# Optimization experiments

Hardware: AMD Instinct MI355X
Metric: run time of the kernel (lower is better)

The kernel has to match this reference:

```python
import jax, jax.numpy as jnp
import numpy as np
import math

H = 14
W = 14
MU_MAX = math.sqrt((H / 2) ** 2 + (W / 2) ** 2)
EPS = 1e-6
LN_EPS = 1e-5


def _distance_sq():
    fy = np.fft.fftfreq(H) * H
    fx = np.fft.rfftfreq(W) * W
    d = fy[:, None] ** 2 + fx[None, :] ** 2  # (H, W//2+1)
    return jnp.asarray(d[None, None], dtype=jnp.float32)  # (1,1,H,W//2+1)


def setup_inputs() -> dict:
    key = jax.random.key(0)
    k0, k1, k2 = jax.random.split(key, 3)
    B, C, HID = 256, 768, 192  # hidden = max(768//4, 8)
    return {
        "x": jax.random.normal(k0, (B, 197, C), jnp.float32),
        "ln_gamma": jnp.ones((C,), jnp.float32),
        "ln_beta": jnp.zeros((C,), jnp.float32),
        "w1": jax.random.normal(k1, (C, HID), jnp.float32) * 0.02,
        "b1": jnp.zeros((HID,), jnp.float32),
        "w2": jax.random.normal(k2, (HID, 2), jnp.float32) * 0.02,
        "b2": jnp.zeros((2,), jnp.float32),
        "residual_scale": jnp.asarray(1e-4, jnp.float32),
    }


def reference(x, ln_gamma, ln_beta, w1, b1, w2, b2, residual_scale):
    b, _, c = x.shape
    cls_tok = x[:, :1]          # (B,1,C)
    xs = x[:, 1:]               # (B,196,C) raw spatial tokens
    # LayerNorm (biased variance, eps=1e-5 like torch default)
    mu_ln = xs.mean(-1, keepdims=True)
    var_ln = xs.var(-1, keepdims=True)
    xn = (xs - mu_ln) / jnp.sqrt(var_ln + LN_EPS) * ln_gamma + ln_beta
    # to (B,C,H,W) grid
    xg = xn.transpose(0, 2, 1).reshape(b, c, H, W)
    xm = xg.mean((-2, -1), keepdims=True)
    spec = jnp.fft.rfft2(xg - xm, norm='ortho')  # (B,C,H,W//2+1) complex
    energy = jnp.log1p(jnp.abs(spec)).mean((-2, -1))  # (B,C)
    hdn = jax.nn.gelu(energy @ w1 + b1, approximate=False)
    out2 = hdn @ w2 + b2  # (B,2)
    mu = jnp.maximum(MU_MAX * jax.nn.sigmoid(out2[:, 0]), 1.0).reshape(b, 1, 1, 1)
    sigma = jnp.maximum(jax.nn.softplus(out2[:, 1]), 0.1).reshape(b, 1, 1, 1)
    mask = jnp.exp(-_distance_sq() / (2.0 * mu ** 2 * sigma + EPS))
    filtered = jnp.fft.irfft2(spec * mask, s=(H, W), norm='ortho') + xm
    toks = filtered.reshape(b, c, H * W).transpose(0, 2, 1)  # (B,196,C)
    delta = toks - xn
    return jnp.concatenate([cls_tok, xs + residual_scale * delta], axis=1)
```

## Files before the change

kernel.cpp:

```cpp
#include <hip/hip_runtime.h>
#include <hip/hip_fp16.h>
#include <math.h>

#define NB    256
#define NTOKP 197
#define NTOK  196
#define NC    768
#define NHID  192
#define NH    14
#define NVF   8
#define CHT   64
#define NTILE 12
#define NCH   8
#define CCH   (NC / NCH)

constexpr float CT14[14] = {
    1.0f, 0.9009688679024191f, 0.6234898018587336f, 0.22252093395631445f,
    -0.22252093395631434f, -0.6234898018587335f, -0.9009688679024191f, -1.0f,
    -0.9009688679024191f, -0.6234898018587335f, -0.22252093395631434f,
    0.22252093395631445f, 0.6234898018587336f, 0.9009688679024191f};
constexpr float ST14[14] = {
    0.0f, 0.4338837391175581f, 0.7818314824680298f, 0.9749279121818236f,
    0.9749279121818236f, 0.7818314824680299f, 0.43388373911755823f, 0.0f,
    -0.43388373911755823f, -0.7818314824680299f, -0.9749279121818236f,
    -0.9749279121818236f, -0.7818314824680298f, -0.4338837391175581f};

__global__ __launch_bounds__(256) void k_stats(const float* __restrict__ x,
                                               float2* __restrict__ msv) {
  int row = blockIdx.x * 4 + (threadIdx.x >> 6);
  int lane = threadIdx.x & 63;
  if (row >= NB * NTOK) return;
  int b = row / NTOK, t = row - b * NTOK;
  const float4* p = (const float4*)(x + ((size_t)b * NTOKP + 1 + t) * NC);
  float s = 0.f, ss = 0.f;
#pragma unroll
  for (int k = 0; k < 3; ++k) {
    float4 v = p[lane + k * 64];
    s += v.x + v.y + v.z + v.w;
    ss += v.x * v.x + v.y * v.y + v.z * v.z + v.w * v.w;
  }
#pragma unroll
  for (int off = 32; off; off >>= 1) {
    s += __shfl_down(s, off);
    ss += __shfl_down(ss, off);
  }
  if (lane == 0) {
    float m = s * (1.f / NC);
    float var = ss * (1.f / NC) - m * m;
    msv[row] = make_float2(m, rsqrtf(var + 1e-5f));
  }
}

__global__ __launch_bounds__(256) void k_fwd(const float* __restrict__ x,
                                             const float* __restrict__ gamma,
                                             const float* __restrict__ beta,
                                             const float2* __restrict__ msv,
                                             float* __restrict__ energy) {
  __shared__ __half2 A[NH * NVF * CHT];
  __shared__ float2 ms[NTOK];
  __shared__ float esum[256];
  int b = blockIdx.y, c0 = blockIdx.x * CHT, tid = threadIdx.x;
  int c = tid & 63, w = tid >> 6;

  for (int k = tid; k < NTOK; k += 256) ms[k] = msv[b * NTOK + k];
  float g = gamma[c0 + c], be = beta[c0 + c];

  __half2 TW1[14], TW2[14];
#pragma unroll
  for (int k = 0; k < 14; ++k) {
    TW1[k] = __floats2half2_rn(CT14[k], -ST14[k]);
    TW2[k] = __floats2half2_rn(ST14[k], CT14[k]);
  }
  __syncthreads();

#pragma unroll 1
  for (int i = w; i < NH; i += 4) {
    const float* xr = x + ((size_t)b * NTOKP + 1 + i * NH) * NC + c0 + c;
    __half2 xh[NH];
#pragma unroll
    for (int j = 0; j < NH; ++j) {
      float2 m = ms[i * NH + j];
      xh[j] = __float2half2_rn((xr[(size_t)j * NC] - m.x) * m.y * g + be);
    }
    __half2 acc[NVF];
#pragma unroll
    for (int v = 0; v < NVF; ++v) acc[v] = __floats2half2_rn(0.f, 0.f);
#pragma unroll
    for (int j = 0; j < NH; ++j) {
#pragma unroll
      for (int v = 0; v < NVF; ++v)
        acc[v] = __hfma2(xh[j], TW1[(v * j) % 14], acc[v]);
    }
#pragma unroll
    for (int v = 0; v < NVF; ++v) A[(i * NVF + v) * CHT + c] = acc[v];
  }
  __syncthreads();

  float part = 0.f;
#pragma unroll 1
  for (int vv = 0; vv < 2; ++vv) {
    int v = w * 2 + vv;
    const __half2* Ac = A + v * CHT + c;
    __half2 S[NH];
#pragma unroll
    for (int u = 0; u < NH; ++u) S[u] = __floats2half2_rn(0.f, 0.f);
#pragma unroll
    for (int i = 0; i < NH; ++i) {
      __half2 a = Ac[i * NVF * CHT];
      __half2 arr = __low2half2(a);
      __half2 aii = __high2half2(a);
#pragma unroll
      for (int u = 0; u < NH; ++u) {
        int k = (u * i) % 14;
        S[u] = __hfma2(arr, TW1[k], __hfma2(aii, TW2[k], S[u]));
      }
    }
#pragma unroll
    for (int u = 0; u < NH; ++u) {
      float2 s = __half22float2(S[u]);
      float m2 = fmaf(s.x, s.x, s.y * s.y);
      part += __logf(1.f + __builtin_amdgcn_sqrtf(m2) * (1.f / 14.f));
    }
    if (w == 0 && vv == 0) {
      part -= __logf(1.f + fabsf(__low2float(S[0])) * (1.f / 14.f));
    }
  }
  esum[tid] = part;
  __syncthreads();
  if (w == 0) {
    float e = esum[c] + esum[c + 64] + esum[c + 128] + esum[c + 192];
    energy[(size_t)b * NC + c0 + c] = e * (1.f / 112.f);
  }
}

__global__ __launch_bounds__(192) void k_mlp1(const float* __restrict__ energy,
                                              const float* __restrict__ w1,
                                              float* __restrict__ partial) {
  int s = blockIdx.x, b = blockIdx.y;
  int h = threadIdx.x;
  const float* ep = energy + (size_t)b * NC + s * CCH;
  const float* wp = w1 + (size_t)s * CCH * NHID + h;
  float acc = 0.f;
#pragma unroll 8
  for (int cc = 0; cc < CCH; ++cc)
    acc = fmaf(ep[cc], wp[(size_t)cc * NHID], acc);
  partial[((size_t)b * NCH + s) * NHID + h] = acc;
}

__global__ __launch_bounds__(192) void k_final(const float* __restrict__ partial,
                                               const float* __restrict__ b1,
                                               const float* __restrict__ w2,
                                               const float* __restrict__ b2,
                                               float* __restrict__ m2s) {
  __shared__ float2 sh[NHID];
  int b = blockIdx.x, h = threadIdx.x;
  float a = b1[h];
#pragma unroll
  for (int s = 0; s < NCH; ++s) a += partial[((size_t)b * NCH + s) * NHID + h];
  float ge = 0.5f * a * (1.f + erff(a * 0.70710678118654752f));
  sh[h] = make_float2(ge * w2[2 * h], ge * w2[2 * h + 1]);
  __syncthreads();
  if (h < 64) {
    float p0 = sh[h].x + sh[h + 64].x + sh[h + 128].x;
    float p1 = sh[h].y + sh[h + 64].y + sh[h + 128].y;
#pragma unroll
    for (int off = 32; off; off >>= 1) {
      p0 += __shfl_down(p0, off);
      p1 += __shfl_down(p1, off);
    }
    if (h == 0) {
      float o0 = p0 + b2[0], o1 = p1 + b2[1];
      float muv = 9.899494936611665f / (1.f + expf(-o0));
      muv = fmaxf(muv, 1.f);
      float sp = (o1 > 20.f) ? o1 : log1pf(expf(o1));
      float sg = fmaxf(sp, 0.1f);
      m2s[b] = 2.f * muv * muv * sg + 1e-6f;
    }
  }
}

__global__ __launch_bounds__(256) void k_inv(const float* __restrict__ x,
                                             const float* __restrict__ gamma,
                                             const float* __restrict__ beta,
                                             const float2* __restrict__ msv,
                                             const float* __restrict__ m2s,
                                             const float* __restrict__ rscale,
                                             float* __restrict__ out) {
  __shared__ __half2 T[NH * 7 * CHT];
  __shared__ float2 ms[NTOK];
  __shared__ float wexp[NH];
  __shared__ float kc[NH];
  int b = blockIdx.y, c0 = blockIdx.x * CHT, tid = threadIdx.x;
  int c = tid & 63, w = tid >> 6;
  float rs = rscale[0];

  for (int k = tid; k < NTOK; k += 256) ms[k] = msv[b * NTOK + k];
  if (tid < CHT) {
    size_t idx = (size_t)b * NTOKP * NC + c0 + tid;
    out[idx] = x[idx];
  }
  float msb = m2s[b];
  if (tid < NH) {
    int f = (tid <= 7) ? tid : 14 - tid;
    wexp[tid] = __expf(-(float)(f * f) / msb);
  }
  __syncthreads();
  if (tid < NH) {
    float s = 0.f;
#pragma unroll
    for (int k = 0; k < NH; ++k) s = fmaf(wexp[k], CT14[(k * tid) % 14], s);
    kc[tid] = s * (1.f / 14.f);
  }
  float g = gamma[c0 + c], be = beta[c0 + c];
  __syncthreads();

  float kr[NH];
#pragma unroll
  for (int d = 0; d < NH; ++d) kr[d] = kc[d];
  __half2 khp[NH];
#pragma unroll
  for (int d = 0; d < NH; ++d) khp[d] = __floats2half2_rn(kr[d], kr[(d + 1) % 14]);

#pragma unroll 1
  for (int i = w; i < NH; i += 4) {
    const float* xr = x + ((size_t)b * NTOKP + 1 + i * NH) * NC + c0 + c;
    __half2 xh[NH];
#pragma unroll
    for (int j = 0; j < NH; ++j) {
      float2 m = ms[i * NH + j];
      xh[j] = __float2half2_rn((xr[(size_t)j * NC] - m.x) * m.y * g + be);
    }
#pragma unroll
    for (int jp = 0; jp < 7; ++jp) {
      __half2 acc = __floats2half2_rn(0.f, 0.f);
#pragma unroll
      for (int j = 0; j < NH; ++j)
        acc = __hfma2(xh[j], khp[(2 * jp - j + 28) % 14], acc);
      T[(i * 7 + jp) * CHT + c] = acc;
    }
  }
  __syncthreads();

#pragma unroll 1
  for (int jq = w; jq < NH; jq += 4) {
    int jp = jq >> 1, hi = jq & 1;
    __half2 acc2[7];
#pragma unroll
    for (int d = 0; d < 7; ++d) acc2[d] = __floats2half2_rn(0.f, 0.f);
#pragma unroll
    for (int i = 0; i < NH; ++i) {
      __half2 t = T[(i * 7 + jp) * CHT + c];
      __half2 yi = hi ? __high2half2(t) : __low2half2(t);
#pragma unroll
      for (int d = 0; d < 7; ++d)
        acc2[d] = __hfma2(yi, khp[(2 * d - i + 28) % 14], acc2[d]);
    }
    const float* xr = x + ((size_t)b * NTOKP + 1 + jq) * NC + c0 + c;
    float* outr = out + ((size_t)b * NTOKP + 1 + jq) * NC + c0 + c;
#pragma unroll
    for (int ii = 0; ii < NH; ++ii) {
      float z = (ii & 1) ? __high2float(acc2[ii >> 1]) : __low2float(acc2[ii >> 1]);
      float xv = xr[(size_t)ii * NH * NC];
      float2 m = ms[ii * NH + jq];
      float xn = (xv - m.x) * m.y * g + be;
      outr[(size_t)ii * NH * NC] = xv + rs * (z - xn);
    }
  }
}

extern "C" void kernel_launch(void* const* d_in, const int* in_sizes, int n_in,
                              void* d_out, int out_size, void* d_ws, size_t ws_size,
                              hipStream_t stream) {
  (void)in_sizes; (void)n_in; (void)out_size; (void)ws_size;
  const float* x      = (const float*)d_in[0];
  const float* gamma  = (const float*)d_in[1];
  const float* beta   = (const float*)d_in[2];
  const float* w1     = (const float*)d_in[3];
  const float* b1     = (const float*)d_in[4];
  const float* w2     = (const float*)d_in[5];
  const float* b2     = (const float*)d_in[6];
  const float* rscale = (const float*)d_in[7];
  float* out = (float*)d_out;

  char* wsb = (char*)d_ws;
  float2* msv    = (float2*)(wsb + 0);
  float* energy  = (float*)(wsb + 401408);
  float* partial = (float*)(wsb + 1187840);
  float* m2s     = (float*)(wsb + 2760704);

  k_stats<<<(NB * NTOK + 3) / 4, 256, 0, stream>>>(x, msv);
  k_fwd<<<dim3(NTILE, NB), 256, 0, stream>>>(x, gamma, beta, msv, energy);
  k_mlp1<<<dim3(NCH, NB), 192, 0, stream>>>(energy, w1, partial);
  k_final<<<NB, 192, 0, stream>>>(partial, b1, w2, b2, m2s);
  k_inv<<<dim3(NTILE, NB), 256, 0, stream>>>(x, gamma, beta, msv, m2s, rscale,
                                             out);
}
```

Baseline: 154.1 us.

## Split column DFT into even/odd halves and batch logs via products

Replaces the direct 14-point complex DFT over rows with a radix-2 decimation (even/odd 7-point sums combined with twiddles), which roughly halves the FMA count. It also exploits Hermitian symmetry for the v=0 and v=7 frequency columns to skip redundant outputs. The per-element log1p calls become a product of (14+|S|) terms followed by two logs, with the constant log(14) offset subtracted at the end. This cuts transcendental work but risks fp32 overflow or precision loss in the products, plus extra half-precision error from the recombination step.

```diff
diff --git a/kernel.cpp b/kernel.cpp
--- a/kernel.cpp
+++ b/kernel.cpp
@@ -100,36 +100,61 @@
 #pragma unroll 1
   for (int vv = 0; vv < 2; ++vv) {
     int v = w * 2 + vv;
+    bool herm = (v == 0) || (v == 7);
     const __half2* Ac = A + v * CHT + c;
-    __half2 S[NH];
-#pragma unroll
-    for (int u = 0; u < NH; ++u) S[u] = __floats2half2_rn(0.f, 0.f);
-#pragma unroll
-    for (int i = 0; i < NH; ++i) {
-      __half2 a = Ac[i * NVF * CHT];
-      __half2 arr = __low2half2(a);
-      __half2 aii = __high2half2(a);
-#pragma unroll
-      for (int u = 0; u < NH; ++u) {
-        int k = (u * i) % 14;
-        S[u] = __hfma2(arr, TW1[k], __hfma2(aii, TW2[k], S[u]));
+    __half2 E[7], O[7];
+#pragma unroll
+    for (int k = 0; k < 7; ++k) {
+      E[k] = __floats2half2_rn(0.f, 0.f);
+      O[k] = __floats2half2_rn(0.f, 0.f);
+    }
+#pragma unroll
+    for (int m = 0; m < 7; ++m) {
+      __half2 ae = Ac[(2 * m) * NVF * CHT];
+      __half2 ao = Ac[(2 * m + 1) * NVF * CHT];
+      __half2 aer = __low2half2(ae), aei = __high2half2(ae);
+      __half2 aor = __low2half2(ao), aoi = __high2half2(ao);
+#pragma unroll
+      for (int k = 0; k < 7; ++k) {
+        int t = (2 * k * m) % 14;
+        E[k] = __hfma2(aer, TW1[t], __hfma2(aei, TW2[t], E[k]));
+        O[k] = __hfma2(aor, TW1[t], __hfma2(aoi, TW2[t], O[k]));
       }
     }
-#pragma unroll
-    for (int u = 0; u < NH; ++u) {
-      float2 s = __half22float2(S[u]);
-      float m2 = fmaf(s.x, s.x, s.y * s.y);
-      part += __logf(1.f + __builtin_amdgcn_sqrtf(m2) * (1.f / 14.f));
-    }
-    if (w == 0 && vv == 0) {
-      part -= __logf(1.f + fabsf(__low2float(S[0])) * (1.f / 14.f));
-    }
+    float pa = 1.f, pb = 1.f;
+#pragma unroll
+    for (int u = 0; u < 14; ++u) {
+      if (!herm || u < 8) {
+        int k = u % 7;
+        __half2 Ov = O[k];
+        __half2 S = __hfma2(__low2half2(Ov), TW1[u],
+                            __hfma2(__high2half2(Ov), TW2[u], E[k]));
+        float2 s2 = __half22float2(S);
+        float mag = 14.f + __builtin_amdgcn_sqrtf(fmaf(s2.x, s2.x, s2.y * s2.y));
+        if (herm) {
+          float msq = mag * mag;
+          if (u == 0) {
+            if (v == 7) pb *= mag;
+          } else if (u <= 3) {
+            pa *= msq;
+          } else if (u <= 6) {
+            pb *= msq;
+          } else {
+            pb *= mag;
+          }
+        } else {
+          if (u < 7) pa *= mag; else pb *= mag;
+        }
+      }
+    }
+    part += __logf(pa) + __logf(pb);
   }
   esum[tid] = part;
   __syncthreads();
   if (w == 0) {
     float e = esum[c] + esum[c + 64] + esum[c + 128] + esum[c + 192];
-    energy[(size_t)b * NC + c0 + c] = e * (1.f / 112.f);
+    energy[(size_t)b * NC + c0 + c] =
+        (e - 111.f * 2.6390573296152584f) * (1.f / 112.f);
   }
 }
 
```

Measured after the change: 144.4 us. -6.3%, faster.
